# Kernel tuning notes

Measured on AMD Instinct MI355X. Metric: run time of the kernel, lower is better.

The kernel has to match this reference:

```python
import jax, jax.numpy as jnp
import numpy as np


def setup_inputs() -> dict:
    key = jax.random.key(0)
    k1, k2 = jax.random.split(key)
    B, F, Ci, R = 16, 1024, 64, 1
    Co, K = 64, 4
    ll = jax.random.normal(k1, (B, F, Ci, R), dtype=jnp.float32)
    logits = jax.random.normal(k2, (Co, Ci, K, K, R), dtype=jnp.float32)
    return {"ll": ll, "logits": logits}


def reference(ll, logits):
    # ll: (B, F, Ci, R)   logits: (Co, Ci, K, K, R)
    B, F, Ci, R = ll.shape
    Co, _, K, _, _ = logits.shape
    H = W = int(F ** 0.5)
    OH, OW = H // K, W // K
    # normalize weights over input channels (sum_dim=1)
    lw = jax.nn.log_softmax(logits, axis=1)  # (Co, Ci, K, K, R)
    # b (h w) ci r -> b ci h w r
    x = ll.reshape(B, H, W, Ci, R).transpose(0, 3, 1, 2, 4)
    # b ci (oh kh) (ow kw) r -> b ci oh ow kh kw r
    x = x.reshape(B, Ci, OH, K, OW, K, R).transpose(0, 1, 2, 4, 3, 5, 6)
    # broadcast-add log-weights (shared over oh, ow) then logsumexp over ci
    weighted = x[:, None] + lw[None, :, :, None, None, :, :, :]  # (B, Co, Ci, OH, OW, K, K, R)
    res = jax.scipy.special.logsumexp(weighted, axis=2)          # (B, Co, OH, OW, K, K, R)
    # b co oh ow kh kw r -> b (oh kh ow kw) co r
    out = res.transpose(0, 2, 4, 3, 5, 1, 6).reshape(B, F, Co, R)
    return out
```

## Files before the change

### kernel.cpp

```cpp
#include <hip/hip_runtime.h>

#define CI 64
#define CO 64
#define F_ 1024
#define KK 4
#define NPAT 16

__device__ float E_buf[NPAT * CI * CO];

__device__ __forceinline__ float bcast(float v, int l) {
    return __int_as_float(__builtin_amdgcn_readlane(__float_as_int(v), l));
}

__global__ __launch_bounds__(256) void prep_kernel(
    const float* __restrict__ logits)
{
    const int pat = blockIdx.x >> 2;
    const int q   = blockIdx.x & 3;
    const int t   = threadIdx.x;
    const int co  = t & 63;
    const int i   = t >> 6;
    #pragma unroll
    for (int k = 0; k < 4; ++k) {
        const int ci = q * 16 + i * 4 + k;
        const float e = __expf(logits[co * (CI * KK * KK) + ci * (KK * KK) + pat]);
        E_buf[pat * (CI * CO) + (ci >> 2) * (CO * 4) + co * 4 + (ci & 3)] = e;
    }
}

__global__ __launch_bounds__(256, 4) void main_kernel(
    const float* __restrict__ ll, float* __restrict__ out)
{
    const int tid   = threadIdx.x;
    const int lane  = tid & 63;
    const int wv    = tid >> 6;
    const int bid   = blockIdx.x;
    const int pat   = bid & (NPAT - 1);
    const int chunk = bid >> 4;
    const int kh = pat >> 2, kw = pat & 3;

    int   idx[4];
    float p[4];
    #pragma unroll
    for (int j = 0; j < 4; ++j) {
        const int pr = (chunk << 4) + (wv << 2) + j;
        const int b  = pr >> 6;
        const int oh = (pr >> 3) & 7;
        const int ow = pr & 7;
        const int f  = (oh * 4 + kh) * 32 + (ow * 4 + kw);
        idx[j] = (b * F_ + f) * CI + lane;
        p[j]   = ll[idx[j]];
    }

    float4 wv4[16];
    const float4* Ep4 = reinterpret_cast<const float4*>(E_buf + pat * (CI * CO)) + lane;
    #pragma unroll
    for (int g = 0; g < 16; ++g) wv4[g] = Ep4[g * CO];
    float wreg[CI];
    #pragma unroll
    for (int g = 0; g < 16; ++g) {
        wreg[4 * g + 0] = wv4[g].x; wreg[4 * g + 1] = wv4[g].y;
        wreg[4 * g + 2] = wv4[g].z; wreg[4 * g + 3] = wv4[g].w;
    }

    float ts[8];
    #pragma unroll
    for (int i = 0; i < 8; ++i)
        ts[i] = (wreg[i] + wreg[i + 8]) + (wreg[i + 16] + wreg[i + 24])
              + (wreg[i + 32] + wreg[i + 40]) + (wreg[i + 48] + wreg[i + 56]);
    const float lsum = __logf(((ts[0] + ts[1]) + (ts[2] + ts[3]))
                            + ((ts[4] + ts[5]) + (ts[6] + ts[7])));

    #pragma unroll
    for (int j = 0; j < 4; ++j) p[j] = __expf(p[j]);

    float a0[4] = {0.f,0.f,0.f,0.f}, a1[4] = {0.f,0.f,0.f,0.f};
    float a2[4] = {0.f,0.f,0.f,0.f}, a3[4] = {0.f,0.f,0.f,0.f};
    #pragma unroll
    for (int ci = 0; ci < CI; ci += 4) {
        #pragma unroll
        for (int j = 0; j < 4; ++j) {
            a0[j] = fmaf(bcast(p[j], ci + 0), wreg[ci + 0], a0[j]);
            a1[j] = fmaf(bcast(p[j], ci + 1), wreg[ci + 1], a1[j]);
            a2[j] = fmaf(bcast(p[j], ci + 2), wreg[ci + 2], a2[j]);
            a3[j] = fmaf(bcast(p[j], ci + 3), wreg[ci + 3], a3[j]);
        }
    }
    #pragma unroll
    for (int j = 0; j < 4; ++j)
        out[idx[j]] = __logf((a0[j] + a1[j]) + (a2[j] + a3[j])) - lsum;
}

extern "C" void kernel_launch(void* const* d_in, const int* in_sizes, int n_in,
                              void* d_out, int out_size, void* d_ws, size_t ws_size,
                              hipStream_t stream) {
    const float* ll     = (const float*)d_in[0];
    const float* logits = (const float*)d_in[1];
    float* out = (float*)d_out;
    (void)d_ws; (void)ws_size;
    prep_kernel<<<dim3(64), dim3(256), 0, stream>>>(logits);
    main_kernel<<<dim3(1024), dim3(256), 0, stream>>>(ll, out);
}
```

Before: 63.94 us.

## Precompute per-pattern log-normalizer in prep and broadcast via ds_bpermute

The prep kernel now runs one block per kernel pattern, writes the exp weights with float4 stores, and reduces them per output channel into a log-sum buffer. The main kernel therefore no longer sums its 64 weight registers and takes a log for every block. The lane broadcast switches from readlane (a scalar-register read) to ds_bpermute with a constant byte address, which goes through the LDS crossbar. The prep grid shrinks from 64 to 16 blocks, which reduces its parallelism, and bpermute has longer latency than readlane.

Result: slower. 65.32 us (+2.2%).

```diff
diff --git a/kernel.cpp b/kernel.cpp
--- a/kernel.cpp
+++ b/kernel.cpp
@@ -7,25 +7,37 @@
 #define NPAT 16
 
 __device__ float E_buf[NPAT * CI * CO];
+__device__ float LS_buf[NPAT * CO];
 
-__device__ __forceinline__ float bcast(float v, int l) {
-    return __int_as_float(__builtin_amdgcn_readlane(__float_as_int(v), l));
+__device__ __forceinline__ float bcast(float v, int ci_byte) {
+    return __int_as_float(__builtin_amdgcn_ds_bpermute(ci_byte, __float_as_int(v)));
 }
 
 __global__ __launch_bounds__(256) void prep_kernel(
     const float* __restrict__ logits)
 {
-    const int pat = blockIdx.x >> 2;
-    const int q   = blockIdx.x & 3;
+    const int pat = blockIdx.x;
     const int t   = threadIdx.x;
     const int co  = t & 63;
     const int i   = t >> 6;
+    float psum = 0.f;
     #pragma unroll
-    for (int k = 0; k < 4; ++k) {
-        const int ci = q * 16 + i * 4 + k;
-        const float e = __expf(logits[co * (CI * KK * KK) + ci * (KK * KK) + pat]);
-        E_buf[pat * (CI * CO) + (ci >> 2) * (CO * 4) + co * 4 + (ci & 3)] = e;
+    for (int g4 = 0; g4 < 4; ++g4) {
+        const int g = i * 4 + g4;
+        float4 e;
+        e.x = __expf(logits[co * (CI * KK * KK) + (4 * g + 0) * (KK * KK) + pat]);
+        e.y = __expf(logits[co * (CI * KK * KK) + (4 * g + 1) * (KK * KK) + pat]);
+        e.z = __expf(logits[co * (CI * KK * KK) + (4 * g + 2) * (KK * KK) + pat]);
+        e.w = __expf(logits[co * (CI * KK * KK) + (4 * g + 3) * (KK * KK) + pat]);
+        *reinterpret_cast<float4*>(&E_buf[pat * (CI * CO) + g * (CO * 4) + co * 4]) = e;
+        psum += (e.x + e.y) + (e.z + e.w);
     }
+    __shared__ float red[4][64];
+    red[i][co] = psum;
+    __syncthreads();
+    if (t < 64)
+        LS_buf[pat * 64 + t] =
+            __logf((red[0][t] + red[1][t]) + (red[2][t] + red[3][t]));
 }
 
 __global__ __launch_bounds__(256, 4) void main_kernel(
@@ -56,20 +68,15 @@
     const float4* Ep4 = reinterpret_cast<const float4*>(E_buf + pat * (CI * CO)) + lane;
     #pragma unroll
     for (int g = 0; g < 16; ++g) wv4[g] = Ep4[g * CO];
+
+    const float lsum = LS_buf[pat * 64 + lane];
+
     float wreg[CI];
     #pragma unroll
     for (int g = 0; g < 16; ++g) {
         wreg[4 * g + 0] = wv4[g].x; wreg[4 * g + 1] = wv4[g].y;
         wreg[4 * g + 2] = wv4[g].z; wreg[4 * g + 3] = wv4[g].w;
     }
-
-    float ts[8];
-    #pragma unroll
-    for (int i = 0; i < 8; ++i)
-        ts[i] = (wreg[i] + wreg[i + 8]) + (wreg[i + 16] + wreg[i + 24])
-              + (wreg[i + 32] + wreg[i + 40]) + (wreg[i + 48] + wreg[i + 56]);
-    const float lsum = __logf(((ts[0] + ts[1]) + (ts[2] + ts[3]))
-                            + ((ts[4] + ts[5]) + (ts[6] + ts[7])));
 
     #pragma unroll
     for (int j = 0; j < 4; ++j) p[j] = __expf(p[j]);
@@ -80,10 +87,10 @@
     for (int ci = 0; ci < CI; ci += 4) {
         #pragma unroll
         for (int j = 0; j < 4; ++j) {
-            a0[j] = fmaf(bcast(p[j], ci + 0), wreg[ci + 0], a0[j]);
-            a1[j] = fmaf(bcast(p[j], ci + 1), wreg[ci + 1], a1[j]);
-            a2[j] = fmaf(bcast(p[j], ci + 2), wreg[ci + 2], a2[j]);
-            a3[j] = fmaf(bcast(p[j], ci + 3), wreg[ci + 3], a3[j]);
+            a0[j] = fmaf(bcast(p[j], 4 * (ci + 0)), wreg[ci + 0], a0[j]);
+            a1[j] = fmaf(bcast(p[j], 4 * (ci + 1)), wreg[ci + 1], a1[j]);
+            a2[j] = fmaf(bcast(p[j], 4 * (ci + 2)), wreg[ci + 2], a2[j]);
+            a3[j] = fmaf(bcast(p[j], 4 * (ci + 3)), wreg[ci + 3], a3[j]);
         }
     }
     #pragma unroll
@@ -98,6 +105,6 @@
     const float* logits = (const float*)d_in[1];
     float* out = (float*)d_out;
     (void)d_ws; (void)ws_size;
-    prep_kernel<<<dim3(64), dim3(256), 0, stream>>>(logits);
+    prep_kernel<<<dim3(16), dim3(256), 0, stream>>>(logits);
     main_kernel<<<dim3(1024), dim3(256), 0, stream>>>(ll, out);
 }
```
